# Optimization experiments

Hardware: AMD Instinct MI355X
Metric: run time of the kernel (lower is better)

The kernel has to match this reference:

```python
import jax, jax.numpy as jnp
import numpy as np
from jax import lax

M_BLOCKS = 4
D = 768
N = 8
L = 2040  # divisible by 1,2,3,4 so every block is full, matching the floor-based slicing


def setup_inputs() -> dict:
    key = jax.random.key(0)
    ks = jax.random.split(key, 7)
    X = jax.random.normal(ks[0], (N, L, D), dtype=jnp.float32)
    # char_mixer: Conv1d(d, d, kernel_size=3, padding='same')
    conv_w = jax.random.normal(ks[1], (D, D, 3), dtype=jnp.float32) * (1.0 / np.sqrt(3 * D))
    conv_b = jax.random.normal(ks[2], (D,), dtype=jnp.float32) * 0.01
    # F_R: Linear(d, 1)
    wr = jax.random.normal(ks[3], (D, 1), dtype=jnp.float32) * (1.0 / np.sqrt(D))
    br = jax.random.normal(ks[4], (1,), dtype=jnp.float32) * 0.01
    # F_D: Linear(d, d)
    wd = jax.random.normal(ks[5], (D, D), dtype=jnp.float32) * (1.0 / np.sqrt(D))
    bd = jax.random.normal(ks[6], (D,), dtype=jnp.float32) * 0.01
    return {"X": X, "conv_w": conv_w, "conv_b": conv_b, "wr": wr, "br": br, "wd": wd, "bd": bd}


def reference(X, conv_w, conv_b, wr, br, wd, bd):
    n, l, d = X.shape
    # char mixer: Conv1d over sequence (NCH layout)
    x = lax.conv_general_dilated(
        X.transpose(0, 2, 1), conv_w, window_strides=(1,), padding='SAME',
        dimension_numbers=('NCH', 'OIH', 'NCH'))
    x = (x + conv_b[None, :, None]).transpose(0, 2, 1)  # (N, L, d)

    # multi-scale block-pooled candidates X_B: (N, L, M, d)
    cands = []
    for b in range(1, M_BLOCKS + 1):  # small fixed loop over block sizes
        xb = x.reshape(n, l // b, b, d).mean(axis=2)       # mean-pool F over each block
        cands.append(jnp.repeat(xb, b, axis=1))            # broadcast block mean to positions
    XB = jnp.stack(cands, axis=2)

    # route scores F_R: Linear(d,1); softmax over trailing size-1 dim (faithful to source)
    P = jax.nn.softmax(XB @ wr + br, axis=-1)              # (N, L, M, 1)

    # calibration: softmax(P P^T) P
    P = P.reshape(n, l, M_BLOCKS)
    A = jax.nn.softmax(jnp.einsum('nlm,nkm->nlk', P, P), axis=-1)  # (N, L, L)
    P = jnp.einsum('nlk,nkm->nlm', A, P)                   # (N, L, M)

    # blend candidates and project with F_D
    X_hat = jnp.einsum('nlm,nlmd->nld', P, XB)             # (N, L, d)
    return X_hat @ wd + bd
```

## Files before the change

kernel.cpp:

```cpp
#include <hip/hip_runtime.h>

#define N_B    8
#define L_SEQ  2040
#define D_DIM  768
#define KDIM   2304
#define M_ROWS 16320
#define LPAD   2042

typedef __bf16 bf16x8 __attribute__((ext_vector_type(8)));
typedef float  f32x4  __attribute__((ext_vector_type(4)));

__device__ __forceinline__ unsigned short f2bf_u(float f) {
  union { float f; unsigned u; } v; v.f = f;
  unsigned u = v.u;
  return (unsigned short)((u + 0x7FFFu + ((u >> 16) & 1u)) >> 16);
}

__device__ __forceinline__ void async16(const unsigned short* g, const unsigned char* l) {
  __builtin_amdgcn_global_load_lds(
      (const __attribute__((address_space(1))) void*)g,
      (__attribute__((address_space(3))) void*)l, 16, 0, 0);
}

__global__ void k_tr2(const float* __restrict__ wd, unsigned short* __restrict__ wdT,
                      const float* __restrict__ cw, unsigned short* __restrict__ cwT) {
  __shared__ float tile[32][33];
  const int z = blockIdx.z;
  const float* in = z ? cw : wd;
  unsigned short* out = z ? cwT : wdT;
  const int R = 768, C = z ? 2304 : 768;
  if (!z && blockIdx.x >= 24) return;
  int tx = threadIdx.x, ty = threadIdx.y;
  int c0 = blockIdx.x * 32;
  int r0 = blockIdx.y * 32;
  for (int i = ty; i < 32; i += 8) {
    int r = r0 + i, c = c0 + tx;
    tile[i][tx] = (r < R && c < C) ? in[(size_t)r * C + c] : 0.f;
  }
  __syncthreads();
  for (int i = ty; i < 32; i += 8) {
    int oc = c0 + i;
    int orr = r0 + tx;
    if (oc < C && orr < R) out[(size_t)oc * R + orr] = f2bf_u(tile[tx][i]);
  }
}

__global__ __launch_bounds__(256) void k_pw(
    const unsigned short* __restrict__ wdT, const unsigned short* __restrict__ cwT,
    unsigned short* __restrict__ Bblk,
    const float* __restrict__ conv_b, const float* __restrict__ wd,
    const float* __restrict__ bd, float* __restrict__ bias2,
    const float* __restrict__ X, unsigned short* __restrict__ Xpad) {
  __shared__ unsigned short sA[128 * 32];
  __shared__ unsigned short sB[128 * 32];
  __shared__ float red[256];
  const int bid = blockIdx.x;
  const int t = threadIdx.x;

  if (bid >= 120) {
    size_t idx = ((size_t)(bid - 120) * 256 + t) * 4;
    const size_t per_n = (size_t)LPAD * D_DIM;
    int n = (int)(idx / per_n);
    size_t rem = idx - (size_t)n * per_n;
    int lp = (int)(rem / D_DIM);
    int d  = (int)(rem - (size_t)lp * D_DIM);
    ushort4 o;
    if (lp == 0 || lp == LPAD - 1) {
      o.x = 0; o.y = 0; o.z = 0; o.w = 0;
    } else {
      const float4 f = *(const float4*)&X[((size_t)n * L_SEQ + (lp - 1)) * D_DIM + d];
      o.x = f2bf_u(f.x); o.y = f2bf_u(f.y); o.z = f2bf_u(f.z); o.w = f2bf_u(f.w);
    }
    *(ushort4*)&Xpad[idx] = o;
    return;
  }

  if (bid >= 108) {
    const int b2 = bid - 108;
    const int o = b2 * 64 + (t & 63);
    const int sl = t >> 6;
    float acc = 0.f;
    for (int dm = sl * 192; dm < sl * 192 + 192; ++dm)
      acc += conv_b[dm] * wd[(size_t)dm * D_DIM + o];
    red[t] = acc;
    __syncthreads();
    if (t < 64)
      bias2[o] = 4.f * (red[t] + red[t + 64] + red[t + 128] + red[t + 192]) + bd[o];
    return;
  }

  const int bm = bid / 18, bn = bid - bm * 18;
  const int lane = t & 63, w = t >> 6;
  const int wr = w >> 1, wc = w & 1;
  const int lr = lane & 15, lg = lane >> 4;

  const int c0 = t, c1 = t + 256;
  const unsigned short* aB0 = wdT + (size_t)(bm * 128 + (c0 >> 2)) * 768 + (c0 & 3) * 8;
  const unsigned short* aB1 = wdT + (size_t)(bm * 128 + (c1 >> 2)) * 768 + (c1 & 3) * 8;
  const unsigned short* bB0 = cwT + (size_t)(bn * 128 + (c0 >> 2)) * 768 + (c0 & 3) * 8;
  const unsigned short* bB1 = cwT + (size_t)(bn * 128 + (c1 >> 2)) * 768 + (c1 & 3) * 8;

  f32x4 acc[4][4] = {};
  int aOff[4], bOff[4];
#pragma unroll
  for (int i = 0; i < 4; ++i) {
    aOff[i] = (wr * 64 + i * 16 + lr) * 4 + lg;
    bOff[i] = (wc * 64 + i * 16 + lr) * 4 + lg;
  }
  const bf16x8* At = (const bf16x8*)sA;
  const bf16x8* Bt = (const bf16x8*)sB;

  for (int kt = 0; kt < 24; ++kt) {
    const int ko = kt * 32;
    __syncthreads();
    async16(aB0 + ko, (const unsigned char*)&sA[c0 * 8]);
    async16(aB1 + ko, (const unsigned char*)&sA[c1 * 8]);
    async16(bB0 + ko, (const unsigned char*)&sB[c0 * 8]);
    async16(bB1 + ko, (const unsigned char*)&sB[c1 * 8]);
    __syncthreads();
    bf16x8 av[4], bv[4];
#pragma unroll
    for (int i = 0; i < 4; ++i) { av[i] = At[aOff[i]]; bv[i] = Bt[bOff[i]]; }
#pragma unroll
    for (int mi = 0; mi < 4; ++mi)
#pragma unroll
      for (int ni = 0; ni < 4; ++ni)
        acc[mi][ni] = __builtin_amdgcn_mfma_f32_16x16x32_bf16(av[mi], bv[ni], acc[mi][ni], 0, 0, 0);
  }

#pragma unroll
  for (int ni = 0; ni < 4; ++ni) {
    const int jp = bn * 128 + wc * 64 + ni * 16 + lr;
    const int di = jp / 3;
    const int kk = jp - di * 3;
    const int j = kk * 768 + di;
    const int kt2 = j >> 6, rem = j & 63;
    const int kh = rem >> 5, o = (rem >> 3) & 3, e = rem & 7;
    const size_t jbase = (size_t)kt2 * 16384 + kh * 8192 + o * 128 + e;
#pragma unroll
    for (int mi = 0; mi < 4; ++mi) {
      const int row0 = bm * 128 + wr * 64 + mi * 16 + lg * 4;
      f32x4 v = acc[mi][ni];
#pragma unroll
      for (int i = 0; i < 4; ++i) {
        const int dd = row0 + i;
        const int p = dd >> 8, cl = dd & 255, blk = cl >> 4, r = cl & 15;
        Bblk[(size_t)p * 589824 + jbase + blk * 512 + r * 8] = f2bf_u(v[i]);
      }
    }
  }
}

__global__ __launch_bounds__(512, 2) void k_conv192(
    const unsigned short* __restrict__ Xpad, const unsigned short* __restrict__ Bblk,
    const float* __restrict__ bias2, float* __restrict__ Y) {
  __shared__ unsigned char lds[114688];

  const int tid = threadIdx.x;
  const int lane = tid & 63;
  const int wid = tid >> 6;
  const int wr = wid >> 2, wc = wid & 3;

  const int bid = blockIdx.x;
  const int xcd = bid & 7, idx = bid >> 3;
  const int swz = (xcd < 7 ? xcd * 32 : 224 + (xcd - 7) * 31) + idx;
  const int bm = swz / 3, bn = swz - bm * 3;

  const unsigned short *aS0, *aS1, *aS2;
  {
#define ACHUNK(rr, dst) { \
    int c = tid + (rr) * 512; \
    int kh = c / 768, q = c - kh * 768; \
    int li = q & 63; \
    int rl = (q >> 6) * 16 + (li & 15); \
    int m = bm * 192 + rl; \
    int n = m / L_SEQ, l = m - n * L_SEQ; \
    dst = Xpad + (size_t)(n * LPAD + l) * D_DIM + kh * 32 + (li >> 4) * 8; }
    ACHUNK(0, aS0) ACHUNK(1, aS1) ACHUNK(2, aS2)
#undef ACHUNK
  }
  const unsigned short* bS = Bblk + (size_t)bn * 589824 + tid * 8;
  const int dA0 = tid * 16, dA1 = dA0 + 8192, dA2 = dA0 + 16384;
  const int dB0 = 24576 + tid * 16, dB1 = dB0 + 8192, dB2 = dB0 + 16384, dB3 = dB0 + 24576;

  const int aRd0 = wr * 6144 + lane * 16;
  const int bRd0 = 24576 + wc * 4096 + lane * 16;

  f32x4 acc[6][4] = {};
  bf16x8 av[6], bv[2];

#define STG(src, koff, dst) async16((src) + (koff), lds + nbb + (dst))
#define LD_AV(kh) \
    _Pragma("unroll") \
    for (int mi = 0; mi < 6; ++mi) \
      av[mi] = *(const bf16x8*)(lds + cb + aRd0 + (kh) * 12288 + mi * 1024);
#define LD_BV(kh, nh) \
    bv[0] = *(const bf16x8*)(lds + cb + bRd0 + (kh) * 16384 + (2 * (nh)) * 1024); \
    bv[1] = *(const bf16x8*)(lds + cb + bRd0 + (kh) * 16384 + (2 * (nh) + 1) * 1024);
#define MF12(nh) \
    __builtin_amdgcn_s_setprio(1); \
    _Pragma("unroll") \
    for (int mi = 0; mi < 6; ++mi) { \
      acc[mi][2 * (nh)]     = __builtin_amdgcn_mfma_f32_16x16x32_bf16(av[mi], bv[0], acc[mi][2 * (nh)], 0, 0, 0); \
      acc[mi][2 * (nh) + 1] = __builtin_amdgcn_mfma_f32_16x16x32_bf16(av[mi], bv[1], acc[mi][2 * (nh) + 1], 0, 0, 0); \
    } \
    __builtin_amdgcn_s_setprio(0);
#define BARR asm volatile("s_barrier" ::: "memory")
#define VM(n) asm volatile("s_waitcnt vmcnt(" #n ")" ::: "memory")
#define LGKM0 asm volatile("s_waitcnt lgkmcnt(0)" ::: "memory")

  {
    const int nbb = 0;
    STG(aS0, 0, dA0); STG(aS1, 0, dA1);
    STG(bS, 0, dB0);  STG(bS, 4096, dB1);
    STG(aS2, 0, dA2);
    STG(bS, 8192, dB2); STG(bS, 12288, dB3);
  }
  VM(3);
  BARR;

  for (int t = 0; t < 36; ++t) {
    const int cb = (t & 1) * 57344;
    const int nbb = ((t & 1) ^ 1) * 57344;
    const bool st = (t < 35);
    const int aoff = (t + 1) * 64;
    const size_t boff = (size_t)(t + 1) * 16384;
    LD_AV(0); LD_BV(0, 0);
    if (st) { STG(aS0, aoff, dA0); STG(aS1, aoff, dA1); }
    BARR;
    MF12(0);
    BARR;
    LD_BV(0, 1);
    if (st) { STG(bS, boff, dB0); STG(bS, boff + 4096, dB1); }
    BARR;
    MF12(1);
    if (st) { VM(4); } else { VM(0); }
    BARR;
    LD_AV(1); LD_BV(1, 0);
    if (st) { STG(aS2, aoff, dA2); STG(bS, boff + 8192, dB2); }
    BARR;
    MF12(0);
    BARR;
    LD_BV(1, 1);
    if (st) { STG(bS, boff + 12288, dB3); }
    BARR;
    MF12(1);
    VM(3);
    BARR;
  }

  const int lr = lane & 15, lg = lane >> 4;
  const f32x4 bias = *(const f32x4*)&bias2[bn * 256 + lane * 4];
#pragma unroll
  for (int p = 0; p < 2; ++p) {
    if (p) { BARR; }
    if (wr == p) {
#pragma unroll
      for (int mi = 0; mi < 6; ++mi)
#pragma unroll
        for (int ni = 0; ni < 4; ++ni)
#pragma unroll
          for (int i = 0; i < 4; ++i)
            *(float*)(lds + ((mi * 16 + lg * 4 + i) * 256 + (wc * 64 + ni * 16 + lr)) * 4) =
                acc[mi][ni][i];
    }
    LGKM0;
    BARR;
    f32x4 y[12];
#pragma unroll
    for (int i = 0; i < 12; ++i)
      y[i] = *(const f32x4*)(lds + ((wid * 12 + i) * 256 + lane * 4) * 4);
    f32x4 m2[6], m3[4], m4[3];
#pragma unroll
    for (int j = 0; j < 6; ++j) m2[j] = (y[2 * j] + y[2 * j + 1]) * 0.5f;
#pragma unroll
    for (int j = 0; j < 4; ++j) m3[j] = (y[3 * j] + y[3 * j + 1] + y[3 * j + 2]) * (1.f / 3.f);
#pragma unroll
    for (int j = 0; j < 3; ++j) m4[j] = (y[4 * j] + y[4 * j + 1] + y[4 * j + 2] + y[4 * j + 3]) * 0.25f;
    const int grow0 = bm * 192 + p * 96 + wid * 12;
#pragma unroll
    for (int i = 0; i < 12; ++i) {
      f32x4 o = y[i] + m2[i >> 1] + m3[i / 3] + m4[i >> 2] + bias;
      *(f32x4*)&Y[(size_t)(grow0 + i) * D_DIM + bn * 256 + lane * 4] = o;
    }
  }
#undef STG
#undef LD_AV
#undef LD_BV
#undef MF12
#undef BARR
#undef VM
#undef LGKM0
}

extern "C" void kernel_launch(void* const* d_in, const int* in_sizes, int n_in,
                              void* d_out, int out_size, void* d_ws, size_t ws_size,
                              hipStream_t stream) {
  const float* X      = (const float*)d_in[0];
  const float* conv_w = (const float*)d_in[1];
  const float* conv_b = (const float*)d_in[2];
  const float* wd     = (const float*)d_in[5];
  const float* bd     = (const float*)d_in[6];
  float* out = (float*)d_out;

  const size_t off_Xpad  = 0;
  const size_t off_wdT   = 25092096;
  const size_t off_cwT   = 26271744;
  const size_t off_Bblk  = 29810688;
  const size_t off_bias2 = 33349632;
  const size_t NEED      = 33352704;
  if (ws_size < NEED) return;

  char* ws = (char*)d_ws;
  unsigned short* Xpad  = (unsigned short*)(ws + off_Xpad);
  unsigned short* wdT   = (unsigned short*)(ws + off_wdT);
  unsigned short* cwT   = (unsigned short*)(ws + off_cwT);
  unsigned short* Bblk  = (unsigned short*)(ws + off_Bblk);
  float*          bias2 = (float*)(ws + off_bias2);

  k_tr2<<<dim3(72, 24, 2), dim3(32, 8), 0, stream>>>(wd, wdT, conv_w, cwT);
  k_pw<<<120 + 12252, 256, 0, stream>>>(wdT, cwT, Bblk, conv_b, wd, bd, bias2, X, Xpad);
  k_conv192<<<255, 512, 0, stream>>>(Xpad, Bblk, bias2, out);
}
```

Measured before the change: 89.84 us.

## Store padded bf16 input in k-chunk-major layout for contiguous A-tile loads

The padded bf16 copy of X is re-laid out as [n][k-chunk of 8][padded row][8], so each 16-byte A-operand load in the conv GEMM reads consecutive rows of one channel chunk instead of striding by the full row width. The conversion pass now has each thread handle 32 channels of one row and write four 16-byte chunks, cutting its grid from 12252 to 1536 blocks. The conv kernel computes per-step A offsets with a small divide-free mapping over the three conv taps. The aim is better coalescing and fewer memory transactions for A staging, at the cost of strided writes in the conversion and extra integer address math per iteration.

```diff
diff --git a/kernel.cpp b/kernel.cpp
--- a/kernel.cpp
+++ b/kernel.cpp
@@ -9,6 +9,7 @@
 
 typedef __bf16 bf16x8 __attribute__((ext_vector_type(8)));
 typedef float  f32x4  __attribute__((ext_vector_type(4)));
+typedef unsigned short ushort8 __attribute__((ext_vector_type(8)));
 
 __device__ __forceinline__ unsigned short f2bf_u(float f) {
   union { float f; unsigned u; } v; v.f = f;
@@ -50,7 +51,7 @@
     unsigned short* __restrict__ Bblk,
     const float* __restrict__ conv_b, const float* __restrict__ wd,
     const float* __restrict__ bd, float* __restrict__ bias2,
-    const float* __restrict__ X, unsigned short* __restrict__ Xpad) {
+    const float* __restrict__ X, unsigned short* __restrict__ Xpad2) {
   __shared__ unsigned short sA[128 * 32];
   __shared__ unsigned short sB[128 * 32];
   __shared__ float red[256];
@@ -58,20 +59,36 @@
   const int t = threadIdx.x;
 
   if (bid >= 120) {
-    size_t idx = ((size_t)(bid - 120) * 256 + t) * 4;
-    const size_t per_n = (size_t)LPAD * D_DIM;
-    int n = (int)(idx / per_n);
-    size_t rem = idx - (size_t)n * per_n;
-    int lp = (int)(rem / D_DIM);
-    int d  = (int)(rem - (size_t)lp * D_DIM);
-    ushort4 o;
-    if (lp == 0 || lp == LPAD - 1) {
-      o.x = 0; o.y = 0; o.z = 0; o.w = 0;
+    const int pb = bid - 120;
+    const int n  = pb / 192;
+    const int r  = pb - n * 192;
+    const int lpT = r / 12, kcT = r - lpT * 12;
+    const int lpi = t & 127, dhalf = t >> 7;
+    const int lp = lpT * 128 + lpi;
+    if (lp >= LPAD) return;
+    const int xrow = lp - 1;
+    const bool zero = (xrow < 0) || (xrow >= L_SEQ);
+    const int di0 = kcT * 64 + dhalf * 32;
+    float f[32];
+    if (!zero) {
+      const f32x4* xs = (const f32x4*)(X + ((size_t)n * L_SEQ + xrow) * D_DIM + di0);
+#pragma unroll
+      for (int i = 0; i < 8; ++i) {
+        f32x4 v = xs[i];
+        f[i * 4 + 0] = v[0]; f[i * 4 + 1] = v[1]; f[i * 4 + 2] = v[2]; f[i * 4 + 3] = v[3];
+      }
     } else {
-      const float4 f = *(const float4*)&X[((size_t)n * L_SEQ + (lp - 1)) * D_DIM + d];
-      o.x = f2bf_u(f.x); o.y = f2bf_u(f.y); o.z = f2bf_u(f.z); o.w = f2bf_u(f.w);
-    }
-    *(ushort4*)&Xpad[idx] = o;
+#pragma unroll
+      for (int i = 0; i < 32; ++i) f[i] = 0.f;
+    }
+#pragma unroll
+    for (int ki = 0; ki < 4; ++ki) {
+      ushort8 o;
+#pragma unroll
+      for (int e = 0; e < 8; ++e) o[e] = f2bf_u(f[ki * 8 + e]);
+      const int kc = kcT * 8 + dhalf * 4 + ki;
+      *(ushort8*)&Xpad2[(((size_t)n * 96 + kc) * LPAD + lp) * 8] = o;
+    }
     return;
   }
 
@@ -152,7 +169,7 @@
 }
 
 __global__ __launch_bounds__(512, 2) void k_conv192(
-    const unsigned short* __restrict__ Xpad, const unsigned short* __restrict__ Bblk,
+    const unsigned short* __restrict__ Xpad2, const unsigned short* __restrict__ Bblk,
     const float* __restrict__ bias2, float* __restrict__ Y) {
   __shared__ unsigned char lds[114688];
 
@@ -166,19 +183,27 @@
   const int swz = (xcd < 7 ? xcd * 32 : 224 + (xcd - 7) * 31) + idx;
   const int bm = swz / 3, bn = swz - bm * 3;
 
-  const unsigned short *aS0, *aS1, *aS2;
+  int aBase0, aBase1, aBase2;
+  int aC0, aC1, aC2;
   {
-#define ACHUNK(rr, dst) { \
+#define ACONST(rr, bout, cout) { \
     int c = tid + (rr) * 512; \
     int kh = c / 768, q = c - kh * 768; \
     int li = q & 63; \
     int rl = (q >> 6) * 16 + (li & 15); \
     int m = bm * 192 + rl; \
     int n = m / L_SEQ, l = m - n * L_SEQ; \
-    dst = Xpad + (size_t)(n * LPAD + l) * D_DIM + kh * 32 + (li >> 4) * 8; }
-    ACHUNK(0, aS0) ACHUNK(1, aS1) ACHUNK(2, aS2)
-#undef ACHUNK
-  }
+    bout = (n * 96 * LPAD + l) * 8; \
+    cout = kh * 4 + (li >> 4); }
+    ACONST(0, aBase0, aC0) ACONST(1, aBase1, aC1) ACONST(2, aBase2, aC2)
+#undef ACONST
+  }
+#define AOFS(base, C, kt) ({ \
+    int K = (kt) * 8 + (C); \
+    int jdiv = (K >= 192) ? 2 : ((K >= 96) ? 1 : 0); \
+    int kc = K - jdiv * 96; \
+    (base) + (kc * LPAD + jdiv) * 8; })
+
   const unsigned short* bS = Bblk + (size_t)bn * 589824 + tid * 8;
   const int dA0 = tid * 16, dA1 = dA0 + 8192, dA2 = dA0 + 16384;
   const int dB0 = 24576 + tid * 16, dB1 = dB0 + 8192, dB2 = dB0 + 16384, dB3 = dB0 + 24576;
@@ -211,9 +236,9 @@
 
   {
     const int nbb = 0;
-    STG(aS0, 0, dA0); STG(aS1, 0, dA1);
+    STG(Xpad2, AOFS(aBase0, aC0, 0), dA0); STG(Xpad2, AOFS(aBase1, aC1, 0), dA1);
     STG(bS, 0, dB0);  STG(bS, 4096, dB1);
-    STG(aS2, 0, dA2);
+    STG(Xpad2, AOFS(aBase2, aC2, 0), dA2);
     STG(bS, 8192, dB2); STG(bS, 12288, dB3);
   }
   VM(3);
@@ -223,10 +248,13 @@
     const int cb = (t & 1) * 57344;
     const int nbb = ((t & 1) ^ 1) * 57344;
     const bool st = (t < 35);
-    const int aoff = (t + 1) * 64;
-    const size_t boff = (size_t)(t + 1) * 16384;
+    const int kt = t + 1;
+    const int ao0 = AOFS(aBase0, aC0, kt);
+    const int ao1 = AOFS(aBase1, aC1, kt);
+    const int ao2 = AOFS(aBase2, aC2, kt);
+    const size_t boff = (size_t)kt * 16384;
     LD_AV(0); LD_BV(0, 0);
-    if (st) { STG(aS0, aoff, dA0); STG(aS1, aoff, dA1); }
+    if (st) { STG(Xpad2, ao0, dA0); STG(Xpad2, ao1, dA1); }
     BARR;
     MF12(0);
     BARR;
@@ -237,7 +265,7 @@
     if (st) { VM(4); } else { VM(0); }
     BARR;
     LD_AV(1); LD_BV(1, 0);
-    if (st) { STG(aS2, aoff, dA2); STG(bS, boff + 8192, dB2); }
+    if (st) { STG(Xpad2, ao2, dA2); STG(bS, boff + 8192, dB2); }
     BARR;
     MF12(0);
     BARR;
@@ -291,6 +319,7 @@
 #undef BARR
 #undef VM
 #undef LGKM0
+#undef AOFS
 }
 
 extern "C" void kernel_launch(void* const* d_in, const int* in_sizes, int n_in,
@@ -312,13 +341,13 @@
   if (ws_size < NEED) return;
 
   char* ws = (char*)d_ws;
-  unsigned short* Xpad  = (unsigned short*)(ws + off_Xpad);
+  unsigned short* Xpad2 = (unsigned short*)(ws + off_Xpad);
   unsigned short* wdT   = (unsigned short*)(ws + off_wdT);
   unsigned short* cwT   = (unsigned short*)(ws + off_cwT);
   unsigned short* Bblk  = (unsigned short*)(ws + off_Bblk);
   float*          bias2 = (float*)(ws + off_bias2);
 
   k_tr2<<<dim3(72, 24, 2), dim3(32, 8), 0, stream>>>(wd, wdT, conv_w, cwT);
-  k_pw<<<120 + 12252, 256, 0, stream>>>(wdT, cwT, Bblk, conv_b, wd, bd, bias2, X, Xpad);
-  k_conv192<<<255, 512, 0, stream>>>(Xpad, Bblk, bias2, out);
-}
+  k_pw<<<120 + 1536, 256, 0, stream>>>(wdT, cwT, Bblk, conv_b, wd, bd, bias2, X, Xpad2);
+  k_conv192<<<255, 512, 0, stream>>>(Xpad2, Bblk, bias2, out);
+}
```

Measured after the change: 94.12 us. +4.8%, slower.
